# Optimization experiments

Hardware: AMD Instinct MI355X
Metric: run time of the kernel (lower is better)

The kernel has to match this reference:

```python
import jax, jax.numpy as jnp
import numpy as np

POOL_LEN = 2
POOL_SIZE = 4  # pool_len**2
NUM_ITERS = 3

def pool_grid(pool_size):
    # grid of relative positions inside the pooling block, row-major, centered at 0
    b = int(np.sqrt(pool_size))
    off = np.arange(b, dtype=np.float32) - (b - 1) / 2.0
    hh, ww = np.meshgrid(off, off, indexing='ij')
    return jnp.asarray(np.stack([hh.ravel(), ww.ravel()], -1))  # (pool_size, 2)

def posevec_to_rotmat(p):
    # p = (cos t, sin t) unit vector -> [[c,-s],[s,c]]
    x, y = p[..., 0], p[..., 1]
    return jnp.stack([jnp.stack([x, -y], -1), jnp.stack([y, x], -1)], -2)

def inverse_pose(p):
    return jnp.stack([p[..., 0], -p[..., 1]], -1)

def space_to_depth(x, b):
    # x: (B,H,W,D,P) -> (B,H/b,W/b,b*b*D,P), depth ordered (h_in_block, w_in_block, d)
    B, H, W, D, P = x.shape
    x = x.reshape(B, H // b, b, W // b, b, D, P).transpose(0, 1, 3, 2, 4, 5, 6)
    return x.reshape(B, H // b, W // b, b * b * D, P)

def capsule_forward(x, a, pose, alpha, beta, lin_w, lin_b, tg1_w, tg2_w):
    B, H, W, Cin = a.shape
    Cout = lin_w.shape[0]
    b, P = POOL_LEN, POOL_SIZE
    Hp, Wp = (H + 1) // b, (W + 1) // b
    a4 = space_to_depth(a[..., None], b)[..., 0].reshape(B, Hp, Wp, P, Cin)
    pose4 = space_to_depth(pose, b).reshape(B, Hp, Wp, P, Cin, 2)
    # mean_per_channel: sum over pool positions, normalize with zero-norm guard
    m = pose4.sum(3)                                            # (B,Hp,Wp,Cin,2)
    n = jnp.linalg.norm(m, axis=-1, keepdims=True)
    means = m / (n + (1.0 - jnp.sign(n)))
    # get_votes: rotate pool positions into the mean frame, generate per-pair thetas
    pp = pool_grid(P).reshape(1, 1, 1, P, 1, 2, 1)
    rot = posevec_to_rotmat(inverse_pose(means))[:, :, :, None]  # (B,Hp,Wp,1,Cin,2,2)
    tpos = jnp.matmul(rot, pp)                                   # (B,Hp,Wp,P,Cin,2,1)
    tpos = jax.lax.stop_gradient(tpos).reshape(-1, Cin * 2)      # detach(); (B*Hp*Wp*P, 2Cin)
    theta = (tpos @ tg1_w.T) @ tg2_w.T                           # (N, Cout*Cin)
    theta = theta.reshape(B, Hp, Wp, P, Cout, Cin).transpose(0, 1, 2, 4, 3, 5)
    s, c = jnp.sin(theta), jnp.cos(theta)
    g = jnp.stack([c, -s, s, c], -1).reshape(B, Hp, Wp, Cout, P, Cin, 2, 2)
    pm = posevec_to_rotmat(pose4[:, :, :, None])                 # (B,Hp,Wp,1,P,Cin,2,2)
    vote = jnp.matmul(pm, g)[..., 0].reshape(B, Hp, Wp, Cout, P * Cin, 2)

    def mean_fn(v, w):
        mu = (v * w[..., None]).sum(-2)                          # (B,Hp,Wp,Cout,2)
        msk = jnp.sign(jnp.abs(mu))                              # elementwise, as original
        return mu / (jnp.linalg.norm(mu, axis=-1, keepdims=True) + (1.0 - msk))

    def dist(p, v):
        return (1.0 - (p[..., None, :] * v).sum(-1)) / 2.0

    a_e = jnp.broadcast_to(a4.reshape(B, Hp, Wp, 1, P * Cin), (B, Hp, Wp, Cout, P * Cin))
    weight = a_e
    pose_o = mean_fn(vote, weight)
    for _ in range(NUM_ITERS):
        weight = (1.0 - dist(pose_o, vote)) * a_e
        pose_o = mean_fn(vote, weight)
    nd = (1.0 - dist(pose_o, vote)) * weight
    w_sum = jnp.sign(jnp.abs(weight)).sum(-1)
    msk = jnp.sign(jnp.abs(w_sum))
    nd = nd.sum(-1) / (w_sum + (1.0 - msk)) * msk
    agreement = jax.nn.sigmoid(alpha.reshape(1, 1, 1, -1) * nd + (beta.reshape(1, 1, 1, -1) - 1.0)) * msk
    # feature max-pool + linear
    xp = space_to_depth(x[..., None], b)[..., 0].reshape(B, Hp, Wp, P, Cin).max(-2)
    xp = xp.reshape(-1, Cin)
    x_out = xp @ lin_w.T + lin_b
    return x_out, agreement, pose_o, xp

def setup_inputs():
    key = jax.random.key(0)
    ks = jax.random.split(key, 8)
    B, H, W, Cin, Cout = 8, 32, 32, 32, 64
    x = jax.random.normal(ks[0], (B, H, W, Cin), jnp.float32)
    a = jax.random.uniform(ks[1], (B, H, W, Cin), jnp.float32)
    pose = jax.random.normal(ks[2], (B, H, W, Cin, 2), jnp.float32)
    pose = pose / jnp.linalg.norm(pose, axis=-1, keepdims=True)  # unit pose vectors
    alpha = jnp.ones((1,), jnp.float32)
    beta = jnp.ones((1,), jnp.float32)
    lin_w = jax.random.normal(ks[3], (Cout, Cin), jnp.float32) * 0.1
    lin_b = jax.random.normal(ks[4], (Cout,), jnp.float32) * 0.1
    tg1_w = jax.random.normal(ks[5], (32, 2 * Cin), jnp.float32) * 0.1
    tg2_w = jax.random.normal(ks[6], (Cout * Cin, 32), jnp.float32) * 0.1
    return {"x": x, "a": a, "pose": pose, "alpha": alpha, "beta": beta,
            "lin_w": lin_w, "lin_b": lin_b, "tg1_w": tg1_w, "tg2_w": tg2_w}

def reference(x, a, pose, alpha, beta, lin_w, lin_b, tg1_w, tg2_w):
    return capsule_forward(x, a, pose, alpha, beta, lin_w, lin_b, tg1_w, tg2_w)
```

## Files before the change

kernel.cpp:

```cpp
#include <hip/hip_runtime.h>
#include <math.h>

#define NSITE 2048

#define OFF_XOUT 0
#define OFF_AGR  (NSITE*64)
#define OFF_POSE (OFF_AGR + NSITE*64)
#define OFF_XP   (OFF_POSE + NSITE*128)

#define WS_META_OFF (NSITE*128)

__device__ __forceinline__ void norm2_guard(float x, float y, float* ox, float* oy) {
    const float n2  = x*x + y*y;
    const float inv = (n2 > 0.f) ? rsqrtf(n2) : 0.f;
    *ox = x*inv; *oy = y*inv;
}

__global__ __launch_bounds__(256) void capsA(
    const float* __restrict__ x, const float* __restrict__ a,
    const float* __restrict__ pose,
    const float* __restrict__ tg1, const float* __restrict__ lin_w,
    const float* __restrict__ lin_b, float* __restrict__ out,
    float* __restrict__ ws)
{
    const int wave = threadIdx.x >> 6, lane = threadIdx.x & 63;
    const int s  = blockIdx.x*4 + wave;
    const int b  = s >> 8, hp = (s >> 4) & 15, wp = s & 15;
    const int ci = lane & 31, p0 = lane >> 5;

    __shared__ float stp[4][4][64];
    __shared__ float xps[4][32];

    const int base = ((b*32 + 2*hp)*32 + 2*wp)*32 + ci;
    const int i0 = base + p0*32;
    const int i1 = base + 1024 + p0*32;
    const float2 pe0 = ((const float2*)pose)[i0];
    const float2 pe1 = ((const float2*)pose)[i1];
    const float  x0  = x[i0], x1 = x[i1];
    const float  a0  = a[i0], a1 = a[i1];

    const float o0x = __shfl_xor(pe0.x, 32, 64);
    const float o0y = __shfl_xor(pe0.y, 32, 64);
    const float o1x = __shfl_xor(pe1.x, 32, 64);
    const float o1y = __shfl_xor(pe1.y, 32, 64);
    const bool first = (p0 == 0);
    const float A0x = first ? pe0.x : o0x,  A1x = first ? o0x : pe0.x;
    const float A2x = first ? pe1.x : o1x,  A3x = first ? o1x : pe1.x;
    const float A0y = first ? pe0.y : o0y,  A1y = first ? o0y : pe0.y;
    const float A2y = first ? pe1.y : o1y,  A3y = first ? o1y : pe1.y;
    float mx = ((A0x + A1x) + A2x) + A3x;
    float my = ((A0y + A1y) + A2y) + A3y;

    float xm = fmaxf(x0, x1);
    xm = fmaxf(xm, __shfl_xor(xm, 32, 64));
    float sa  = a0 + a1;
    float cnt = (a0 != 0.f ? 1.f : 0.f) + (a1 != 0.f ? 1.f : 0.f);
    sa  += __shfl_xor(sa,  32, 64);
    cnt += __shfl_xor(cnt, 32, 64);
    #pragma unroll
    for (int m = 1; m <= 16; m <<= 1) {
        sa  += __shfl_xor(sa,  m, 64);
        cnt += __shfl_xor(cnt, m, 64);
    }
    if (lane == 0) ((float2*)(ws + WS_META_OFF))[s] = make_float2(sa, cnt);
    if (p0 == 0) {
        out[OFF_XP + s*32 + ci] = xm;
        xps[wave][ci] = xm;
    }

    {
        const float n   = sqrtf(mx*mx + my*my);
        const float den = n + (n == 0.f ? 1.f : 0.f);
        mx /= den; my /= den;
    }

    {
        const float ww_ = (float)p0 - 0.5f;
        const float t0x = -0.5f*mx + my*ww_;
        const float t0y =  0.5f*my + mx*ww_;
        const float t1x =  0.5f*mx + my*ww_;
        const float t1y = -0.5f*my + mx*ww_;
        ((float2*)stp[wave][p0    ])[ci] = make_float2(t0x, t0y);
        ((float2*)stp[wave][p0 + 2])[ci] = make_float2(t1x, t1y);
    }
    __syncthreads();

    {
        const float4* w4 = (const float4*)(tg1 + ci*64);
        const float4* r0 = (const float4*)stp[wave][p0];
        const float4* r1 = (const float4*)stp[wave][p0 + 2];
        float h0 = 0.f, h1 = 0.f;
        #pragma unroll
        for (int k = 0; k < 16; ++k) {
            const float4 wv = w4[k], u = r0[k], v = r1[k];
            h0 += wv.x*u.x + wv.y*u.y + wv.z*u.z + wv.w*u.w;
            h1 += wv.x*v.x + wv.y*v.y + wv.z*v.z + wv.w*v.w;
        }
        ws[s*128 + p0*32 + ci]       = h0;
        ws[s*128 + (p0 + 2)*32 + ci] = h1;
    }

    {
        float acc = lin_b[lane];
        const float4* lw = (const float4*)(lin_w + lane*32);
        const float4* xv = (const float4*)xps[wave];
        #pragma unroll
        for (int k = 0; k < 8; ++k) {
            const float4 wv = lw[k], u = xv[k];
            acc += wv.x*u.x + wv.y*u.y + wv.z*u.z + wv.w*u.w;
        }
        out[OFF_XOUT + s*64 + lane] = acc;
    }
}

__global__ __launch_bounds__(256) void capsB(
    const float* __restrict__ a, const float* __restrict__ pose,
    const float* __restrict__ tg2, const float* __restrict__ ws,
    const float* __restrict__ alpha, const float* __restrict__ beta,
    float* __restrict__ out)
{
    const int g    = blockIdx.x;
    const int sb   = blockIdx.y;
    const int tid  = threadIdx.x;
    const int wave = tid >> 6, lane = tid & 63;
    const int co   = g*8 + wave*2 + (lane >> 5);
    const int ci   = lane & 31;

    float4 r[8];
    {
        const float4* rp = (const float4*)(tg2 + (co*32 + ci)*32);
        #pragma unroll
        for (int k = 0; k < 8; ++k) r[k] = rp[k];
    }
    const float alp = alpha[0];
    const float bet = beta[0] - 1.0f;
    const float2* ws_meta = (const float2*)(ws + WS_META_OFF);

    const int s0 = sb*8;
    for (int s = s0; s < s0 + 8; ++s) {
        const float4* h4 = (const float4*)(ws + s*128);
        float th0 = 0.f, th1 = 0.f, th2 = 0.f, th3 = 0.f;
        #pragma unroll
        for (int k = 0; k < 8; ++k) {
            const float4 rk = r[k];
            const float4 ha = h4[k];
            const float4 hb = h4[8  + k];
            const float4 hc = h4[16 + k];
            const float4 hd = h4[24 + k];
            th0 += rk.x*ha.x + rk.y*ha.y + rk.z*ha.z + rk.w*ha.w;
            th1 += rk.x*hb.x + rk.y*hb.y + rk.z*hb.z + rk.w*hb.w;
            th2 += rk.x*hc.x + rk.y*hc.y + rk.z*hc.z + rk.w*hc.w;
            th3 += rk.x*hd.x + rk.y*hd.y + rk.z*hd.z + rk.w*hd.w;
        }
        const float th[4] = {th0, th1, th2, th3};

        const int b   = s >> 8, hpi = (s >> 4) & 15, wpi = s & 15;
        const int base = ((b*32 + 2*hpi)*32 + 2*wpi)*32 + ci;

        float Sx = 0.f, Sy = 0.f, Sxx = 0.f, Sxy = 0.f, Syy = 0.f;
        #pragma unroll
        for (int p = 0; p < 4; ++p) {
            const int idx = base + (p >> 1)*1024 + (p & 1)*32;
            const float2 pe = ((const float2*)pose)[idx];
            const float  av = a[idx];
            float sn, cs;
            __sincosf(th[p], &sn, &cs);
            const float vx = pe.x*cs - pe.y*sn;
            const float vy = pe.y*cs + pe.x*sn;
            const float ax = av*vx, ay = av*vy;
            Sx += ax; Sy += ay;
            Sxx += ax*vx; Sxy += ax*vy; Syy += ay*vy;
        }
        #pragma unroll
        for (int m = 1; m <= 16; m <<= 1) {
            Sx  += __shfl_xor(Sx,  m, 64);
            Sy  += __shfl_xor(Sy,  m, 64);
            Sxx += __shfl_xor(Sxx, m, 64);
            Sxy += __shfl_xor(Sxy, m, 64);
            Syy += __shfl_xor(Syy, m, 64);
        }

        float px, py;
        norm2_guard(Sx, Sy, &px, &py);
        float qx = px, qy = py;
        #pragma unroll
        for (int it = 0; it < 3; ++it) {
            qx = px; qy = py;
            const float mx = Sx + px*Sxx + py*Sxy;
            const float my = Sy + px*Sxy + py*Syy;
            norm2_guard(mx, my, &px, &py);
        }
        const float2 meta = ws_meta[s];
        const float nd_sum = 0.25f*(meta.x + (px + qx)*Sx + (py + qy)*Sy
                           + px*qx*Sxx + (px*qy + py*qx)*Sxy + py*qy*Syy);
        const float wsum = meta.y;
        const float msk  = (wsum != 0.f) ? 1.f : 0.f;
        const float nd   = nd_sum / (wsum + (1.f - msk)) * msk;
        const float z    = alp*nd + bet;
        const float agr  = msk / (1.f + __expf(-z));

        if ((lane & 31) == 0) {
            out[OFF_AGR  + s*64  + co]       = agr;
            out[OFF_POSE + s*128 + co*2]     = px;
            out[OFF_POSE + s*128 + co*2 + 1] = py;
        }
    }
}

extern "C" void kernel_launch(void* const* d_in, const int* in_sizes, int n_in,
                              void* d_out, int out_size, void* d_ws, size_t ws_size,
                              hipStream_t stream) {
    const float* x     = (const float*)d_in[0];
    const float* a     = (const float*)d_in[1];
    const float* pose  = (const float*)d_in[2];
    const float* alpha = (const float*)d_in[3];
    const float* beta  = (const float*)d_in[4];
    const float* lin_w = (const float*)d_in[5];
    const float* lin_b = (const float*)d_in[6];
    const float* tg1   = (const float*)d_in[7];
    const float* tg2   = (const float*)d_in[8];
    float* out = (float*)d_out;
    float* ws  = (float*)d_ws;

    capsA<<<NSITE/4, 256, 0, stream>>>(x, a, pose, tg1, lin_w, lin_b, out, ws);
    capsB<<<dim3(8, NSITE/8), 256, 0, stream>>>(a, pose, tg2, ws, alpha, beta, out);
}
```

Measured before the change: 144.4 us.

## Fuse site-prep and routing kernels, recomputing hidden projections per block in LDS

Merges the two kernels into one launch. Each block now recomputes the pose means, the first theta-generator projection and the activation metadata for its 8 sites into shared memory, so the workspace round trip through global memory and the second launch go away. The cost is redundancy: the 8 output-channel groups all repeat the same prep work, which adds loads and ALU per block. Only group 0 writes x_out and xp. The prep also adds two block-wide barriers per site pair before the routing loop can start.

```diff
diff --git a/kernel.cpp b/kernel.cpp
--- a/kernel.cpp
+++ b/kernel.cpp
@@ -7,8 +7,6 @@
 #define OFF_AGR  (NSITE*64)
 #define OFF_POSE (OFF_AGR + NSITE*64)
 #define OFF_XP   (OFF_POSE + NSITE*128)
-
-#define WS_META_OFF (NSITE*128)
 
 __device__ __forceinline__ void norm2_guard(float x, float y, float* ox, float* oy) {
     const float n2  = x*x + y*y;
@@ -16,106 +14,11 @@
     *ox = x*inv; *oy = y*inv;
 }
 
-__global__ __launch_bounds__(256) void capsA(
+__global__ __launch_bounds__(256) void caps_fused2(
     const float* __restrict__ x, const float* __restrict__ a,
     const float* __restrict__ pose,
     const float* __restrict__ tg1, const float* __restrict__ lin_w,
-    const float* __restrict__ lin_b, float* __restrict__ out,
-    float* __restrict__ ws)
-{
-    const int wave = threadIdx.x >> 6, lane = threadIdx.x & 63;
-    const int s  = blockIdx.x*4 + wave;
-    const int b  = s >> 8, hp = (s >> 4) & 15, wp = s & 15;
-    const int ci = lane & 31, p0 = lane >> 5;
-
-    __shared__ float stp[4][4][64];
-    __shared__ float xps[4][32];
-
-    const int base = ((b*32 + 2*hp)*32 + 2*wp)*32 + ci;
-    const int i0 = base + p0*32;
-    const int i1 = base + 1024 + p0*32;
-    const float2 pe0 = ((const float2*)pose)[i0];
-    const float2 pe1 = ((const float2*)pose)[i1];
-    const float  x0  = x[i0], x1 = x[i1];
-    const float  a0  = a[i0], a1 = a[i1];
-
-    const float o0x = __shfl_xor(pe0.x, 32, 64);
-    const float o0y = __shfl_xor(pe0.y, 32, 64);
-    const float o1x = __shfl_xor(pe1.x, 32, 64);
-    const float o1y = __shfl_xor(pe1.y, 32, 64);
-    const bool first = (p0 == 0);
-    const float A0x = first ? pe0.x : o0x,  A1x = first ? o0x : pe0.x;
-    const float A2x = first ? pe1.x : o1x,  A3x = first ? o1x : pe1.x;
-    const float A0y = first ? pe0.y : o0y,  A1y = first ? o0y : pe0.y;
-    const float A2y = first ? pe1.y : o1y,  A3y = first ? o1y : pe1.y;
-    float mx = ((A0x + A1x) + A2x) + A3x;
-    float my = ((A0y + A1y) + A2y) + A3y;
-
-    float xm = fmaxf(x0, x1);
-    xm = fmaxf(xm, __shfl_xor(xm, 32, 64));
-    float sa  = a0 + a1;
-    float cnt = (a0 != 0.f ? 1.f : 0.f) + (a1 != 0.f ? 1.f : 0.f);
-    sa  += __shfl_xor(sa,  32, 64);
-    cnt += __shfl_xor(cnt, 32, 64);
-    #pragma unroll
-    for (int m = 1; m <= 16; m <<= 1) {
-        sa  += __shfl_xor(sa,  m, 64);
-        cnt += __shfl_xor(cnt, m, 64);
-    }
-    if (lane == 0) ((float2*)(ws + WS_META_OFF))[s] = make_float2(sa, cnt);
-    if (p0 == 0) {
-        out[OFF_XP + s*32 + ci] = xm;
-        xps[wave][ci] = xm;
-    }
-
-    {
-        const float n   = sqrtf(mx*mx + my*my);
-        const float den = n + (n == 0.f ? 1.f : 0.f);
-        mx /= den; my /= den;
-    }
-
-    {
-        const float ww_ = (float)p0 - 0.5f;
-        const float t0x = -0.5f*mx + my*ww_;
-        const float t0y =  0.5f*my + mx*ww_;
-        const float t1x =  0.5f*mx + my*ww_;
-        const float t1y = -0.5f*my + mx*ww_;
-        ((float2*)stp[wave][p0    ])[ci] = make_float2(t0x, t0y);
-        ((float2*)stp[wave][p0 + 2])[ci] = make_float2(t1x, t1y);
-    }
-    __syncthreads();
-
-    {
-        const float4* w4 = (const float4*)(tg1 + ci*64);
-        const float4* r0 = (const float4*)stp[wave][p0];
-        const float4* r1 = (const float4*)stp[wave][p0 + 2];
-        float h0 = 0.f, h1 = 0.f;
-        #pragma unroll
-        for (int k = 0; k < 16; ++k) {
-            const float4 wv = w4[k], u = r0[k], v = r1[k];
-            h0 += wv.x*u.x + wv.y*u.y + wv.z*u.z + wv.w*u.w;
-            h1 += wv.x*v.x + wv.y*v.y + wv.z*v.z + wv.w*v.w;
-        }
-        ws[s*128 + p0*32 + ci]       = h0;
-        ws[s*128 + (p0 + 2)*32 + ci] = h1;
-    }
-
-    {
-        float acc = lin_b[lane];
-        const float4* lw = (const float4*)(lin_w + lane*32);
-        const float4* xv = (const float4*)xps[wave];
-        #pragma unroll
-        for (int k = 0; k < 8; ++k) {
-            const float4 wv = lw[k], u = xv[k];
-            acc += wv.x*u.x + wv.y*u.y + wv.z*u.z + wv.w*u.w;
-        }
-        out[OFF_XOUT + s*64 + lane] = acc;
-    }
-}
-
-__global__ __launch_bounds__(256) void capsB(
-    const float* __restrict__ a, const float* __restrict__ pose,
-    const float* __restrict__ tg2, const float* __restrict__ ws,
+    const float* __restrict__ lin_b, const float* __restrict__ tg2,
     const float* __restrict__ alpha, const float* __restrict__ beta,
     float* __restrict__ out)
 {
@@ -123,6 +26,104 @@
     const int sb   = blockIdx.y;
     const int tid  = threadIdx.x;
     const int wave = tid >> 6, lane = tid & 63;
+
+    __shared__ float hs[8*128];
+    __shared__ float meta_s[8*2];
+    __shared__ float stp[4][4][64];
+    __shared__ float xps[4][32];
+
+    {
+        const int ci = lane & 31, p0 = lane >> 5;
+        #pragma unroll
+        for (int si = 0; si < 2; ++si) {
+            const int sl = wave*2 + si;
+            const int s  = sb*8 + sl;
+            const int b  = s >> 8, hp = (s >> 4) & 15, wp = s & 15;
+
+            const int base = ((b*32 + 2*hp)*32 + 2*wp)*32 + ci;
+            const int i0 = base + p0*32;
+            const int i1 = base + 1024 + p0*32;
+            const float2 pe0 = ((const float2*)pose)[i0];
+            const float2 pe1 = ((const float2*)pose)[i1];
+            const float  x0  = x[i0], x1 = x[i1];
+            const float  a0  = a[i0], a1 = a[i1];
+
+            const float o0x = __shfl_xor(pe0.x, 32, 64);
+            const float o0y = __shfl_xor(pe0.y, 32, 64);
+            const float o1x = __shfl_xor(pe1.x, 32, 64);
+            const float o1y = __shfl_xor(pe1.y, 32, 64);
+            const bool first = (p0 == 0);
+            const float A0x = first ? pe0.x : o0x,  A1x = first ? o0x : pe0.x;
+            const float A2x = first ? pe1.x : o1x,  A3x = first ? o1x : pe1.x;
+            const float A0y = first ? pe0.y : o0y,  A1y = first ? o0y : pe0.y;
+            const float A2y = first ? pe1.y : o1y,  A3y = first ? o1y : pe1.y;
+            float mx = ((A0x + A1x) + A2x) + A3x;
+            float my = ((A0y + A1y) + A2y) + A3y;
+
+            float xm = fmaxf(x0, x1);
+            xm = fmaxf(xm, __shfl_xor(xm, 32, 64));
+            float sa  = a0 + a1;
+            float cnt = (a0 != 0.f ? 1.f : 0.f) + (a1 != 0.f ? 1.f : 0.f);
+            sa  += __shfl_xor(sa,  32, 64);
+            cnt += __shfl_xor(cnt, 32, 64);
+            #pragma unroll
+            for (int m = 1; m <= 16; m <<= 1) {
+                sa  += __shfl_xor(sa,  m, 64);
+                cnt += __shfl_xor(cnt, m, 64);
+            }
+            if (lane == 0) { meta_s[sl*2] = sa; meta_s[sl*2 + 1] = cnt; }
+            if (p0 == 0) {
+                xps[wave][ci] = xm;
+                if (g == 0) out[OFF_XP + s*32 + ci] = xm;
+            }
+
+            {
+                const float n   = sqrtf(mx*mx + my*my);
+                const float den = n + (n == 0.f ? 1.f : 0.f);
+                mx /= den; my /= den;
+            }
+
+            {
+                const float ww_ = (float)p0 - 0.5f;
+                const float t0x = -0.5f*mx + my*ww_;
+                const float t0y =  0.5f*my + mx*ww_;
+                const float t1x =  0.5f*mx + my*ww_;
+                const float t1y = -0.5f*my + mx*ww_;
+                ((float2*)stp[wave][p0    ])[ci] = make_float2(t0x, t0y);
+                ((float2*)stp[wave][p0 + 2])[ci] = make_float2(t1x, t1y);
+            }
+            __syncthreads();
+
+            {
+                const float4* w4 = (const float4*)(tg1 + ci*64);
+                const float4* r0 = (const float4*)stp[wave][p0];
+                const float4* r1 = (const float4*)stp[wave][p0 + 2];
+                float h0 = 0.f, h1 = 0.f;
+                #pragma unroll
+                for (int k = 0; k < 16; ++k) {
+                    const float4 wv = w4[k], u = r0[k], v = r1[k];
+                    h0 += wv.x*u.x + wv.y*u.y + wv.z*u.z + wv.w*u.w;
+                    h1 += wv.x*v.x + wv.y*v.y + wv.z*v.z + wv.w*v.w;
+                }
+                hs[sl*128 + p0*32 + ci]       = h0;
+                hs[sl*128 + (p0 + 2)*32 + ci] = h1;
+            }
+
+            if (g == 0) {
+                float acc = lin_b[lane];
+                const float4* lw = (const float4*)(lin_w + lane*32);
+                const float4* xv = (const float4*)xps[wave];
+                #pragma unroll
+                for (int k = 0; k < 8; ++k) {
+                    const float4 wv = lw[k], u = xv[k];
+                    acc += wv.x*u.x + wv.y*u.y + wv.z*u.z + wv.w*u.w;
+                }
+                out[OFF_XOUT + s*64 + lane] = acc;
+            }
+            __syncthreads();
+        }
+    }
+
     const int co   = g*8 + wave*2 + (lane >> 5);
     const int ci   = lane & 31;
 
@@ -134,11 +135,10 @@
     }
     const float alp = alpha[0];
     const float bet = beta[0] - 1.0f;
-    const float2* ws_meta = (const float2*)(ws + WS_META_OFF);
-
-    const int s0 = sb*8;
-    for (int s = s0; s < s0 + 8; ++s) {
-        const float4* h4 = (const float4*)(ws + s*128);
+
+    for (int sl = 0; sl < 8; ++sl) {
+        const int s = sb*8 + sl;
+        const float4* h4 = (const float4*)(hs + sl*128);
         float th0 = 0.f, th1 = 0.f, th2 = 0.f, th3 = 0.f;
         #pragma unroll
         for (int k = 0; k < 8; ++k) {
@@ -190,10 +190,11 @@
             const float my = Sy + px*Sxy + py*Syy;
             norm2_guard(mx, my, &px, &py);
         }
-        const float2 meta = ws_meta[s];
-        const float nd_sum = 0.25f*(meta.x + (px + qx)*Sx + (py + qy)*Sy
+        const float sa_s  = meta_s[sl*2];
+        const float cnt_s = meta_s[sl*2 + 1];
+        const float nd_sum = 0.25f*(sa_s + (px + qx)*Sx + (py + qy)*Sy
                            + px*qx*Sxx + (px*qy + py*qx)*Sxy + py*qy*Syy);
-        const float wsum = meta.y;
+        const float wsum = cnt_s;
         const float msk  = (wsum != 0.f) ? 1.f : 0.f;
         const float nd   = nd_sum / (wsum + (1.f - msk)) * msk;
         const float z    = alp*nd + bet;
@@ -220,8 +221,8 @@
     const float* tg1   = (const float*)d_in[7];
     const float* tg2   = (const float*)d_in[8];
     float* out = (float*)d_out;
-    float* ws  = (float*)d_ws;
-
-    capsA<<<NSITE/4, 256, 0, stream>>>(x, a, pose, tg1, lin_w, lin_b, out, ws);
-    capsB<<<dim3(8, NSITE/8), 256, 0, stream>>>(a, pose, tg2, ws, alpha, beta, out);
+    (void)d_ws; (void)ws_size;
+
+    caps_fused2<<<dim3(8, NSITE/8), 256, 0, stream>>>(
+        x, a, pose, tg1, lin_w, lin_b, tg2, alpha, beta, out);
 }
```

Result: slower. 161.2 us (+11.6%).
